# Kernel tuning notes

Measured on AMD Instinct MI355X. Metric: run time of the kernel, lower is better.

## Reference

```python
import jax, jax.numpy as jnp
import numpy as np

N_BUILDINGS = 4096
NUM_CLUSTERS = 128
EMBED_DIM = 128
TEMPORAL_DIM = 24


def setup_inputs() -> dict:
    key = jax.random.key(0)
    ks = jax.random.split(key, 12)
    E, N, C, T = EMBED_DIM, N_BUILDINGS, NUM_CLUSTERS, TEMPORAL_DIM

    def lin(k, fi, fo):
        k1, k2 = jax.random.split(k)
        w = jax.random.normal(k1, (fo, fi), jnp.float32) / np.sqrt(fi).astype(np.float32)
        b = jax.random.normal(k2, (fo,), jnp.float32) * 0.01
        return w, b

    fp_w1, fp_b1 = lin(ks[0], 2 * E + 2, 128)
    fp_w2, fp_b2 = lin(ks[1], 128, 64)
    fp_w3, fp_b3 = lin(ks[2], 64, 1)
    en_w1, en_b1 = lin(ks[3], 1, 16)
    en_w2, en_b2 = lin(ks[4], 16, 1)
    ps_w1, ps_b1 = lin(ks[5], E, 32)
    ps_w2, ps_b2 = lin(ks[6], 32, 1)

    embeddings = jax.random.normal(ks[7], (1, N, E), jnp.float32)
    generation = jax.random.uniform(ks[8], (1, N, T), jnp.float32) * 50.0
    consumption = jax.random.uniform(ks[9], (1, N, T), jnp.float32) * 50.0
    positions = jax.random.uniform(ks[10], (1, N, 2), jnp.float32) * 1000.0
    cluster_assignments = (jnp.arange(N) % C)[None, :].astype(jnp.int32)

    return dict(embeddings=embeddings, generation=generation, consumption=consumption,
                positions=positions,
                fp_w1=fp_w1, fp_b1=fp_b1, fp_w2=fp_w2, fp_b2=fp_b2, fp_w3=fp_w3, fp_b3=fp_b3,
                en_w1=en_w1, en_b1=en_b1, en_w2=en_w2, en_b2=en_b2,
                ps_w1=ps_w1, ps_b1=ps_b1, ps_w2=ps_w2, ps_b2=ps_b2,
                cluster_assignments=cluster_assignments, num_clusters=C, current_hour=12)


def _greedy_cluster(net0, prio, effm, pf):
    """Greedy allocation within one cluster. net0,prio: [K]; effm,pf: [K,K].
    Surplus rows and deficit cols are both visited in descending priority order;
    non-surplus rows have avail=0 and non-deficit cols have needed<=0, matching the
    original code's subset selection + break/continue semantics."""
    K = net0.shape[0]
    order = jnp.argsort(-prio)
    inv = jnp.argsort(order)
    net_o = net0[order]
    eff_o = effm[order][:, order]
    pf_o = pf[order][:, order]

    def outer(dnet, i):
        avail0 = jnp.maximum(net_o[i], 0.0)  # surplus net is never mutated

        def inner(carry, j):
            avail, dn = carry
            needed = -dn[j]
            active = (avail > 0.0) & (needed > 0.0)
            f = jnp.where(active, jnp.minimum(jnp.minimum(avail, needed), pf_o[i, j]), 0.0)
            dn = dn.at[j].add(f * eff_o[i, j])  # deficit receives delivered flow
            return (avail - f, dn), (f, active)

        (_, dnet), (frow, arow) = jax.lax.scan(inner, (avail0, dnet), jnp.arange(K))
        return dnet, (frow, arow)

    dnet, (flows_o, act_o) = jax.lax.scan(outer, net_o, jnp.arange(K))
    return flows_o[inv][:, inv], act_o[inv][:, inv], dnet[inv]


def _forward(embeddings, generation, consumption, positions,
             fp_w1, fp_b1, fp_w2, fp_b2, fp_w3, fp_b3,
             en_w1, en_b1, en_w2, en_b2,
             ps_w1, ps_b1, ps_w2, ps_b2,
             cluster_assignments, num_clusters, current_hour):
    B, N, E = embeddings.shape
    C = num_clusters
    K = N // C
    net = generation[0, :, current_hour] - consumption[0, :, current_hour]  # [N]

    g = jnp.argsort(cluster_assignments[0]).reshape(C, K)  # [C,K] building ids per cluster
    emb_c = embeddings[0][g]   # [C,K,E]
    pos_c = positions[0][g]    # [C,K,2]
    net_c = net[g]             # [C,K]

    # priority scorer (eval mode)
    h = jax.nn.relu(emb_c @ ps_w1.T + ps_b1)
    prio_c = jax.nn.sigmoid(h @ ps_w2.T + ps_b2)[..., 0]  # [C,K]

    # pairwise distances within cluster
    dist = jnp.linalg.norm(pos_c[:, :, None, :] - pos_c[:, None, :, :], axis=-1)  # [C,K,K]

    # efficiency net: eff = 0.85 + 0.13*sigmoid(MLP(dist/1000))
    eh = jax.nn.relu((dist / 1000.0)[..., None] * en_w1[:, 0] + en_b1)  # [C,K,K,16]
    eff = 0.85 + 0.13 * jax.nn.sigmoid(eh @ en_w2.T + en_b2)[..., 0]    # [C,K,K]

    # flow predictor on concat([emb_i, emb_j, dist, hour/24]); split W1 to avoid
    # materializing the [C,K,K,2E+2] feature tensor. Dropout is eval-mode identity.
    W1a, W1b = fp_w1[:, :E], fp_w1[:, E:2 * E]
    w1d, w1h = fp_w1[:, 2 * E], fp_w1[:, 2 * E + 1]
    hi = emb_c @ W1a.T  # [C,K,128]
    hj = emb_c @ W1b.T  # [C,K,128]
    hour_f = current_hour / 24.0
    h1 = jax.nn.relu(hi[:, :, None, :] + hj[:, None, :, :] + dist[..., None] * w1d + hour_f * w1h + fp_b1)
    h2 = jax.nn.relu(h1 @ fp_w2.T + fp_b2)
    pflow = jax.nn.softplus(h2 @ fp_w3.T + fp_b3)[..., 0]  # [C,K,K]

    flows_c, act_c, dnet_c = jax.vmap(_greedy_cluster)(net_c, prio_c, eff, pflow)

    sharing = jnp.zeros((N, N), embeddings.dtype).at[g[:, :, None], g[:, None, :]].set(flows_c)
    effmat = jnp.ones((N, N), embeddings.dtype).at[g[:, :, None], g[:, None, :]].set(
        jnp.where(act_c, eff, 1.0))
    net_after = jnp.zeros((N,), embeddings.dtype).at[g].set(dnet_c)

    sharing = sharing[None]
    effmat = effmat[None]
    total_shared = sharing.sum()
    energy_sent = sharing.sum(axis=2)
    energy_received = (sharing * effmat).sum(axis=1)
    return sharing, effmat, total_shared, energy_sent, energy_received, net_after[None]


def reference(embeddings, generation, consumption, positions,
              fp_w1, fp_b1, fp_w2, fp_b2, fp_w3, fp_b3,
              en_w1, en_b1, en_w2, en_b2,
              ps_w1, ps_b1, ps_w2, ps_b2,
              cluster_assignments, num_clusters, current_hour):
    return _forward(embeddings, generation, consumption, positions,
                    fp_w1, fp_b1, fp_w2, fp_b2, fp_w3, fp_b3,
                    en_w1, en_b1, en_w2, en_b2,
                    ps_w1, ps_b1, ps_w2, ps_b2,
                    cluster_assignments, num_clusters, current_hour)
```

## Files before the change

### kernel.cpp

```cpp
#include <hip/hip_runtime.h>
#include <math.h>

#define NB 4096
#define NC 128
#define NK 32
#define NE 128

typedef __bf16 bf16x8 __attribute__((ext_vector_type(8)));
typedef float floatx4 __attribute__((ext_vector_type(4)));

__device__ __forceinline__ float sigmoidf_(float x){
  if (x >= 0.f){ float z = expf(-x); return 1.f/(1.f+z); }
  float z = expf(x); return z/(1.f+z);
}
__device__ __forceinline__ float softplusf_(float x){
  return fmaxf(x, 0.f) + log1pf(expf(-fabsf(x)));
}
__device__ __forceinline__ unsigned int pack_bf16(float a, float b){
  unsigned short ua = __builtin_bit_cast(unsigned short, (__bf16)a);
  unsigned short ub = __builtin_bit_cast(unsigned short, (__bf16)b);
  return (unsigned int)ua | ((unsigned int)ub << 16);
}

__global__ void k_hijprio(const float* __restrict__ emb, const float* __restrict__ gen,
                          const float* __restrict__ cons, const float* __restrict__ fp_w1,
                          const float* __restrict__ fp_b1, const float* __restrict__ fp_w2,
                          const float* __restrict__ ps_w1, const float* __restrict__ ps_b1,
                          const float* __restrict__ ps_w2, const float* __restrict__ ps_b2,
                          const int* __restrict__ assign, const int* __restrict__ hourp,
                          float* __restrict__ hi, float* __restrict__ hj,
                          float* __restrict__ net, float* __restrict__ prio,
                          int* __restrict__ g, int* __restrict__ row_of,
                          float* __restrict__ w1d_c, float* __restrict__ bzc,
                          uint4* __restrict__ w2f, float* __restrict__ total){
  int bid = blockIdx.x;
  int t = threadIdx.x;
  if (bid < 512){
    __shared__ float es[8*132];
    __shared__ float wsm[128*33];
    __shared__ float wa_s[128*33];
    __shared__ float wb_s[128*33];
    int i0 = bid*8;
    for (int idx = t; idx < 8*128; idx += 256){
      int b = idx >> 7, e = idx & 127;
      es[b*132 + e] = emb[(i0 + b)*128 + e];
    }
    for (int idx = t; idx < 4096; idx += 256){
      int q = idx >> 7, e = idx & 127;
      wsm[e*33 + q] = ps_w1[q*128 + e];
    }
    int o = t & 127, half = t >> 7;
    float ai[4], aj[4];
#pragma unroll
    for (int r = 0; r < 4; ++r){ ai[r] = 0.f; aj[r] = 0.f; }
    for (int ch = 0; ch < 4; ++ch){
      int ec = ch << 5;
      if (ch) __syncthreads();
      for (int idx = t; idx < 4096; idx += 256){
        int row = idx >> 5, e2 = idx & 31;
        wa_s[row*33 + e2] = fp_w1[row*258 + ec + e2];
        wb_s[row*33 + e2] = fp_w1[row*258 + 128 + ec + e2];
      }
      __syncthreads();
      const float* war = &wa_s[o*33];
      const float* wbr = &wb_s[o*33];
#pragma unroll
      for (int e2 = 0; e2 < 32; e2 += 4){
        float wa0 = war[e2+0], wa1 = war[e2+1], wa2 = war[e2+2], wa3 = war[e2+3];
        float wb0 = wbr[e2+0], wb1 = wbr[e2+1], wb2 = wbr[e2+2], wb3 = wbr[e2+3];
        int e = ec + e2;
#pragma unroll
        for (int r = 0; r < 4; ++r){
          float4 ev = *(const float4*)&es[(half*4 + r)*132 + e];
          ai[r] = fmaf(ev.x, wa0, fmaf(ev.y, wa1, fmaf(ev.z, wa2, fmaf(ev.w, wa3, ai[r]))));
          aj[r] = fmaf(ev.x, wb0, fmaf(ev.y, wb1, fmaf(ev.z, wb2, fmaf(ev.w, wb3, aj[r]))));
        }
      }
    }
#pragma unroll
    for (int r = 0; r < 4; ++r){
      int b = i0 + half*4 + r;
      hi[b*128 + o] = ai[r];
      hj[b*128 + o] = aj[r];
    }
    {
      int bl = t >> 5, q = t & 31;
      int i = i0 + bl;
      float acc = ps_b1[q];
      const float* er = &es[bl*132];
      for (int e = 0; e < 128; ++e) acc = fmaf(er[e], wsm[e*33 + q], acc);
      float v = fmaxf(acc, 0.f) * ps_w2[q];
      for (int m = 16; m >= 1; m >>= 1) v += __shfl_xor(v, m, 32);
      if (q == 0){
        prio[i] = sigmoidf_(v + ps_b2[0]);
        int h = hourp[0];
        net[i] = gen[i*24 + h] - cons[i*24 + h];
      }
    }
  } else if (bid < 528){
    __shared__ int hist[NC];
    __shared__ int loc[256];
    int start = (bid - 512)*256;
    for (int c = t; c < NC; c += 256) hist[c] = 0;
    __syncthreads();
    for (int j = t; j < start; j += 256) atomicAdd(&hist[assign[j]], 1);
    int i = start + t;
    int c = assign[i];
    loc[t] = c;
    __syncthreads();
    int r = hist[c];
    for (int j = 0; j < 256; ++j) r += (j < t && loc[j] == c) ? 1 : 0;
    if (r >= NK) r = NK - 1;
    g[c*NK + r] = i;
    row_of[i] = c*NK + r;
  } else if (bid == 528){
    if (t < 128){
      float hour_f = (float)hourp[0] / 24.0f;
      w1d_c[t] = fp_w1[t*258 + 256];
      bzc[t]   = fmaf(hour_f, fp_w1[t*258 + 257], fp_b1[t]);
    }
    if (t == 128) total[0] = 0.f;
  } else {
    for (int ff = t; ff < 1024; ff += 256){
      int lane = ff & 63, fi = ff >> 6;
      int nt = fi >> 2, ks = fi & 3;
      int o = nt*16 + (lane & 15);
      int kb = ks*32 + (lane >> 4)*8;
      const float* src = fp_w2 + o*128 + kb;
      uint4 u;
      u.x = pack_bf16(src[0], src[1]);
      u.y = pack_bf16(src[2], src[3]);
      u.z = pack_bf16(src[4], src[5]);
      u.w = pack_bf16(src[6], src[7]);
      w2f[ff] = u;
    }
  }
}

__global__ __launch_bounds__(512) void k_pfgreedy(
    const float* __restrict__ hi, const float* __restrict__ hj,
    const float* __restrict__ pos, const float* __restrict__ net,
    const float* __restrict__ prio, const float* __restrict__ w1d_c,
    const float* __restrict__ bzc, const uint4* __restrict__ w2f,
    const float* __restrict__ fp_b2, const float* __restrict__ fp_w3,
    const float* __restrict__ fp_b3, const float* __restrict__ en_w1,
    const float* __restrict__ en_b1, const float* __restrict__ en_w2,
    const float* __restrict__ en_b2, const int* __restrict__ g,
    float* __restrict__ fl_c, float* __restrict__ ef_c, float* __restrict__ total,
    float* __restrict__ esent, float* __restrict__ erecv, float* __restrict__ nafter){
  __shared__ float pf_s[1024];
  __shared__ float ef_s[1024];
  __shared__ float fl_s[1024];
  __shared__ float efa_s[1024];
  __shared__ float px[32], py[32];
  __shared__ int gl[32];
  __shared__ int order_s[32];
  int t = threadIdx.x;
  int lane = t & 63, wv = t >> 6;
  int c = blockIdx.x;
  if (t < 32){
    int b = g[c*NK + t];
    gl[t] = b;
    px[t] = pos[2*b];
    py[t] = pos[2*b + 1];
  }
  __syncthreads();
  {
    int l16 = lane & 15, quad = lane >> 4;
    bf16x8 bfr[4][4];
#pragma unroll
    for (int nt = 0; nt < 4; ++nt)
#pragma unroll
      for (int ks = 0; ks < 4; ++ks)
        bfr[nt][ks] = __builtin_bit_cast(bf16x8, w2f[(nt*4 + ks)*64 + lane]);
    float b2v[4], w3v[4];
#pragma unroll
    for (int nt = 0; nt < 4; ++nt){
      b2v[nt] = fp_b2[nt*16 + l16];
      w3v[nt] = fp_w3[nt*16 + l16];
    }
    float b3 = fp_b3[0];
    const float4* wd4 = (const float4*)w1d_c;
    const float4* bz4 = (const float4*)bzc;
    for (int it = 0; it < 8; ++it){
      int tile = it*8 + wv;
      int i = tile >> 1, j0 = (tile & 1)*16;
      int j = j0 + l16;
      float dx = px[i] - px[j], dy = py[i] - py[j];
      float d = sqrtf(fmaf(dx, dx, dy*dy));
      const float4* hi4 = (const float4*)(hi + gl[i]*128);
      const float4* hj4 = (const float4*)(hj + gl[j]*128);
      bf16x8 af[4];
#pragma unroll
      for (int ks = 0; ks < 4; ++ks){
        int q8 = ks*8 + quad*2;
        float4 a0 = hi4[q8], a1 = hi4[q8 + 1];
        float4 b0 = hj4[q8], b1 = hj4[q8 + 1];
        float4 w0 = wd4[q8], w1 = wd4[q8 + 1];
        float4 z0 = bz4[q8], z1 = bz4[q8 + 1];
        float v0 = fmaxf(a0.x + b0.x + fmaf(d, w0.x, z0.x), 0.f);
        float v1 = fmaxf(a0.y + b0.y + fmaf(d, w0.y, z0.y), 0.f);
        float v2 = fmaxf(a0.z + b0.z + fmaf(d, w0.z, z0.z), 0.f);
        float v3 = fmaxf(a0.w + b0.w + fmaf(d, w0.w, z0.w), 0.f);
        float v4 = fmaxf(a1.x + b1.x + fmaf(d, w1.x, z1.x), 0.f);
        float v5 = fmaxf(a1.y + b1.y + fmaf(d, w1.y, z1.y), 0.f);
        float v6 = fmaxf(a1.z + b1.z + fmaf(d, w1.z, z1.z), 0.f);
        float v7 = fmaxf(a1.w + b1.w + fmaf(d, w1.w, z1.w), 0.f);
        uint4 u;
        u.x = pack_bf16(v0, v1);
        u.y = pack_bf16(v2, v3);
        u.z = pack_bf16(v4, v5);
        u.w = pack_bf16(v6, v7);
        af[ks] = __builtin_bit_cast(bf16x8, u);
      }
      floatx4 acc[4];
#pragma unroll
      for (int nt = 0; nt < 4; ++nt){
        acc[nt] = (floatx4){0.f, 0.f, 0.f, 0.f};
#pragma unroll
        for (int ks = 0; ks < 4; ++ks)
          acc[nt] = __builtin_amdgcn_mfma_f32_16x16x32_bf16(af[ks], bfr[nt][ks], acc[nt], 0, 0, 0);
      }
#pragma unroll
      for (int r = 0; r < 4; ++r){
        float s = 0.f;
#pragma unroll
        for (int nt = 0; nt < 4; ++nt)
          s = fmaf(fmaxf(acc[nt][r] + b2v[nt], 0.f), w3v[nt], s);
#pragma unroll
        for (int m = 8; m >= 1; m >>= 1) s += __shfl_xor(s, m);
        if (l16 == 0)
          pf_s[i*32 + j0 + quad*4 + r] = softplusf_(s + b3);
      }
    }
  }
  for (int e = t; e < 1024; e += 512){
    int ii = e >> 5, jj = e & 31;
    float dx = px[ii] - px[jj], dy = py[ii] - py[jj];
    float d = sqrtf(fmaf(dx, dx, dy*dy));
    float ds = d * (1.0f/1000.0f);
    float acc = en_b2[0];
#pragma unroll
    for (int q = 0; q < 16; ++q)
      acc = fmaf(fmaxf(fmaf(ds, en_w1[q], en_b1[q]), 0.f), en_w2[q], acc);
    ef_s[e] = 0.85f + 0.13f*sigmoidf_(acc);
  }
  if (t < 64){
    int tl = t & 31;
    float pr = (t < 32) ? prio[gl[t]] : -1e30f;
    int rank = 0;
    for (int k = 0; k < 32; ++k){
      float pk = __shfl(pr, k, 32);
      rank += ((pk > pr) || (pk == pr && k < tl)) ? 1 : 0;
    }
    if (t < 32) order_s[rank] = t;
  }
  __syncthreads();
  if (t < 64){
    int tl = t & 31;
    int b = order_s[tl];
    float net0 = net[gl[b]];
    float dnet = net0;
    float recv = 0.f;
    for (int i = 0; i < 32; ++i){
      int a = order_s[i];
      float av0 = fmaxf(__shfl(net0, i, 32), 0.f);
      float pf = pf_s[a*32 + b];
      float ef = ef_s[a*32 + b];
      float needed = -dnet;
      float m = (needed > 0.f) ? fminf(needed, pf) : 0.f;
      float s = m;
#pragma unroll
      for (int dd = 1; dd < 32; dd <<= 1){
        float u = __shfl_up(s, dd, 32);
        if (tl >= dd) s += u;
      }
      float Se = __shfl_up(s, 1, 32);
      if (tl == 0) Se = 0.f;
      float rprev = fmaxf(av0 - Se, 0.f);
      int act = (rprev > 0.f) && (needed > 0.f);
      float f = fminf(m, rprev);
      dnet = fmaf(f, ef, dnet);
      recv = fmaf(f, ef, recv);
      if (t < 32){
        fl_s[a*32 + b]  = f;
        efa_s[a*32 + b] = act ? ef : 1.0f;
      }
    }
    if (t < 32){
      nafter[gl[b]] = dnet;
      erecv[gl[b]]  = recv;
    }
  }
  __syncthreads();
  for (int e = t; e < 1024; e += 512){
    fl_c[c*1024 + e] = fl_s[e];
    ef_c[c*1024 + e] = efa_s[e];
  }
  if (t < 32){
    float rs = 0.f;
#pragma unroll
    for (int j = 0; j < 32; ++j)
      rs += fl_s[t*32 + ((j + t) & 31)];
    esent[gl[t]] = rs;
    float cs = rs;
    for (int m = 16; m >= 1; m >>= 1) cs += __shfl_xor(cs, m, 32);
    if (t == 0) atomicAdd(total, cs);
  }
}

__global__ __launch_bounds__(256) void k_write(
    const float* __restrict__ fl_c, const float* __restrict__ ef_c,
    const int* __restrict__ g, const int* __restrict__ row_of,
    float* __restrict__ sharing, float* __restrict__ effm){
  __shared__ float rowS[4096];
  __shared__ float rowE[4096];
  __shared__ int   cols[32];
  __shared__ float vals[32];
  __shared__ float vale[32];
  int t = threadIdx.x;
  int r = blockIdx.x;
  int ra = row_of[r];
  int c = ra >> 5, a = ra & 31;
  if (t < 32){
    cols[t] = g[c*NK + t];
    vals[t] = fl_c[c*1024 + a*32 + t];
    vale[t] = ef_c[c*1024 + a*32 + t];
  }
  float4 z4 = make_float4(0.f, 0.f, 0.f, 0.f);
  float4 o4 = make_float4(1.f, 1.f, 1.f, 1.f);
  float4* s4 = (float4*)rowS;
  float4* e4 = (float4*)rowE;
#pragma unroll
  for (int q = 0; q < 4; ++q){ s4[t + 256*q] = z4; e4[t + 256*q] = o4; }
  __syncthreads();
  if (t < 32){ rowS[cols[t]] = vals[t]; rowE[cols[t]] = vale[t]; }
  __syncthreads();
  const floatx4* s4v = (const floatx4*)rowS;
  const floatx4* e4v = (const floatx4*)rowE;
  floatx4* gs = (floatx4*)(sharing + (long)r*NB);
  floatx4* ge = (floatx4*)(effm    + (long)r*NB);
#pragma unroll
  for (int q = 0; q < 4; ++q){
    __builtin_nontemporal_store(s4v[t + 256*q], &gs[t + 256*q]);
    __builtin_nontemporal_store(e4v[t + 256*q], &ge[t + 256*q]);
  }
}

extern "C" void kernel_launch(void* const* d_in, const int* in_sizes, int n_in,
                              void* d_out, int out_size, void* d_ws, size_t ws_size,
                              hipStream_t stream){
  (void)in_sizes; (void)n_in; (void)out_size; (void)ws_size;
  const float* emb   = (const float*)d_in[0];
  const float* gen   = (const float*)d_in[1];
  const float* cons  = (const float*)d_in[2];
  const float* pos   = (const float*)d_in[3];
  const float* fp_w1 = (const float*)d_in[4];
  const float* fp_b1 = (const float*)d_in[5];
  const float* fp_w2 = (const float*)d_in[6];
  const float* fp_b2 = (const float*)d_in[7];
  const float* fp_w3 = (const float*)d_in[8];
  const float* fp_b3 = (const float*)d_in[9];
  const float* en_w1 = (const float*)d_in[10];
  const float* en_b1 = (const float*)d_in[11];
  const float* en_w2 = (const float*)d_in[12];
  const float* en_b2 = (const float*)d_in[13];
  const float* ps_w1 = (const float*)d_in[14];
  const float* ps_b1 = (const float*)d_in[15];
  const float* ps_w2 = (const float*)d_in[16];
  const float* ps_b2 = (const float*)d_in[17];
  const int*   assign = (const int*)d_in[18];
  const int*   hourp  = (const int*)d_in[20];

  char* ws = (char*)d_ws;
  int*   g      = (int*)  (ws + 0);
  int*   row_of = (int*)  (ws + 16384);
  float* net    = (float*)(ws + 32768);
  float* prio   = (float*)(ws + 49152);
  float* w1d_c  = (float*)(ws + 65536);
  float* bzc    = (float*)(ws + 66048);
  uint4* w2f    = (uint4*)(ws + 131072);
  float* hi     = (float*)(ws + 262144);
  float* hj     = (float*)(ws + 2359296);
  float* fl_c   = (float*)(ws + 4456448);
  float* ef_c   = (float*)(ws + 4980736);

  float* sharing = (float*)d_out;
  float* effm    = sharing + (long)NB*NB;
  float* total   = effm + (long)NB*NB;
  float* esent   = total + 1;
  float* erecv   = esent + NB;
  float* nafter  = erecv + NB;

  hipLaunchKernelGGL(k_hijprio, dim3(530), dim3(256), 0, stream,
                     emb, gen, cons, fp_w1, fp_b1, fp_w2, ps_w1, ps_b1, ps_w2, ps_b2,
                     assign, hourp, hi, hj, net, prio, g, row_of, w1d_c, bzc, w2f, total);
  hipLaunchKernelGGL(k_pfgreedy, dim3(128), dim3(512), 0, stream,
                     hi, hj, pos, net, prio, w1d_c, bzc, w2f, fp_b2, fp_w3, fp_b3,
                     en_w1, en_b1, en_w2, en_b2, g,
                     fl_c, ef_c, total, esent, erecv, nafter);
  hipLaunchKernelGGL(k_write, dim3(4096), dim3(256), 0, stream,
                     fl_c, ef_c, g, row_of, sharing, effm);
}
```

Before: 256.4 us.

## Split pairwise-flow MLP and greedy allocation into separate kernels with doubled grid

```diff
diff --git a/kernel.cpp b/kernel.cpp
--- a/kernel.cpp
+++ b/kernel.cpp
@@ -137,27 +137,20 @@
   }
 }
 
-__global__ __launch_bounds__(512) void k_pfgreedy(
+__global__ __launch_bounds__(512) void k_pflow(
     const float* __restrict__ hi, const float* __restrict__ hj,
-    const float* __restrict__ pos, const float* __restrict__ net,
-    const float* __restrict__ prio, const float* __restrict__ w1d_c,
+    const float* __restrict__ pos, const float* __restrict__ w1d_c,
     const float* __restrict__ bzc, const uint4* __restrict__ w2f,
     const float* __restrict__ fp_b2, const float* __restrict__ fp_w3,
     const float* __restrict__ fp_b3, const float* __restrict__ en_w1,
     const float* __restrict__ en_b1, const float* __restrict__ en_w2,
     const float* __restrict__ en_b2, const int* __restrict__ g,
-    float* __restrict__ fl_c, float* __restrict__ ef_c, float* __restrict__ total,
-    float* __restrict__ esent, float* __restrict__ erecv, float* __restrict__ nafter){
-  __shared__ float pf_s[1024];
-  __shared__ float ef_s[1024];
-  __shared__ float fl_s[1024];
-  __shared__ float efa_s[1024];
+    float* __restrict__ pf_g, float* __restrict__ ef_g){
   __shared__ float px[32], py[32];
   __shared__ int gl[32];
-  __shared__ int order_s[32];
   int t = threadIdx.x;
   int lane = t & 63, wv = t >> 6;
-  int c = blockIdx.x;
+  int c = blockIdx.x >> 1, hb = blockIdx.x & 1;
   if (t < 32){
     int b = g[c*NK + t];
     gl[t] = b;
@@ -182,8 +175,8 @@
     float b3 = fp_b3[0];
     const float4* wd4 = (const float4*)w1d_c;
     const float4* bz4 = (const float4*)bzc;
-    for (int it = 0; it < 8; ++it){
-      int tile = it*8 + wv;
+    for (int it = 0; it < 4; ++it){
+      int tile = hb*32 + it*8 + wv;
       int i = tile >> 1, j0 = (tile & 1)*16;
       int j = j0 + l16;
       float dx = px[i] - px[j], dy = py[i] - py[j];
@@ -230,11 +223,12 @@
 #pragma unroll
         for (int m = 8; m >= 1; m >>= 1) s += __shfl_xor(s, m);
         if (l16 == 0)
-          pf_s[i*32 + j0 + quad*4 + r] = softplusf_(s + b3);
-      }
-    }
-  }
-  for (int e = t; e < 1024; e += 512){
+          pf_g[c*1024 + i*32 + j0 + quad*4 + r] = softplusf_(s + b3);
+      }
+    }
+  }
+  {
+    int e = hb*512 + t;
     int ii = e >> 5, jj = e & 31;
     float dx = px[ii] - px[jj], dy = py[ii] - py[jj];
     float d = sqrtf(fmaf(dx, dx, dy*dy));
@@ -243,8 +237,28 @@
 #pragma unroll
     for (int q = 0; q < 16; ++q)
       acc = fmaf(fmaxf(fmaf(ds, en_w1[q], en_b1[q]), 0.f), en_w2[q], acc);
-    ef_s[e] = 0.85f + 0.13f*sigmoidf_(acc);
-  }
+    ef_g[c*1024 + e] = 0.85f + 0.13f*sigmoidf_(acc);
+  }
+}
+
+__global__ __launch_bounds__(256) void k_greedy(
+    const float* __restrict__ net, const float* __restrict__ prio,
+    const int* __restrict__ g, const float* __restrict__ pf_g,
+    const float* __restrict__ ef_g,
+    float* __restrict__ fl_c, float* __restrict__ ef_c, float* __restrict__ total,
+    float* __restrict__ esent, float* __restrict__ erecv, float* __restrict__ nafter){
+  __shared__ float pf_s[1024];
+  __shared__ float ef_s[1024];
+  __shared__ float fl_s[1024];
+  __shared__ float efa_s[1024];
+  __shared__ int gl[32];
+  __shared__ int order_s[32];
+  int t = threadIdx.x;
+  int c = blockIdx.x;
+  if (t < 32) gl[t] = g[c*NK + t];
+  ((float4*)pf_s)[t] = ((const float4*)(pf_g + c*1024))[t];
+  ((float4*)ef_s)[t] = ((const float4*)(ef_g + c*1024))[t];
+  __syncthreads();
   if (t < 64){
     int tl = t & 31;
     float pr = (t < 32) ? prio[gl[t]] : -1e30f;
@@ -293,7 +307,7 @@
     }
   }
   __syncthreads();
-  for (int e = t; e < 1024; e += 512){
+  for (int e = t; e < 1024; e += 256){
     fl_c[c*1024 + e] = fl_s[e];
     ef_c[c*1024 + e] = efa_s[e];
   }
@@ -384,6 +398,8 @@
   float* hj     = (float*)(ws + 2359296);
   float* fl_c   = (float*)(ws + 4456448);
   float* ef_c   = (float*)(ws + 4980736);
+  float* pf_g   = (float*)(ws + 5505024);
+  float* ef_g   = (float*)(ws + 6029312);
 
   float* sharing = (float*)d_out;
   float* effm    = sharing + (long)NB*NB;
@@ -395,9 +411,11 @@
   hipLaunchKernelGGL(k_hijprio, dim3(530), dim3(256), 0, stream,
                      emb, gen, cons, fp_w1, fp_b1, fp_w2, ps_w1, ps_b1, ps_w2, ps_b2,
                      assign, hourp, hi, hj, net, prio, g, row_of, w1d_c, bzc, w2f, total);
-  hipLaunchKernelGGL(k_pfgreedy, dim3(128), dim3(512), 0, stream,
-                     hi, hj, pos, net, prio, w1d_c, bzc, w2f, fp_b2, fp_w3, fp_b3,
-                     en_w1, en_b1, en_w2, en_b2, g,
+  hipLaunchKernelGGL(k_pflow, dim3(256), dim3(512), 0, stream,
+                     hi, hj, pos, w1d_c, bzc, w2f, fp_b2, fp_w3, fp_b3,
+                     en_w1, en_b1, en_w2, en_b2, g, pf_g, ef_g);
+  hipLaunchKernelGGL(k_greedy, dim3(128), dim3(256), 0, stream,
+                     net, prio, g, pf_g, ef_g,
                      fl_c, ef_c, total, esent, erecv, nafter);
   hipLaunchKernelGGL(k_write, dim3(4096), dim3(256), 0, stream,
                      fl_c, ef_c, g, row_of, sharing, effm);
```

Result: faster. 246.2 us (-4.0%).
